# Kernel optimization log

Hardware: AMD Instinct MI355X
Metric: run time of the kernel (lower is better)

## Reference

```python
import jax, jax.numpy as jnp
import numpy as np

INPUT_DIM = 16
LW = 128          # layerwidth
NB_LAYERS = 4
NB_X = 4096
NB_THETA = 128
PARAM_COUNT = INPUT_DIM * LW + LW + (NB_LAYERS - 1) * (LW * LW + LW) + LW + 1  # 51841


def setup_inputs() -> dict:
    k1, k2 = jax.random.split(jax.random.key(0))
    x = jax.random.normal(k1, (NB_X, INPUT_DIM), dtype=jnp.float32)
    theta = jax.random.normal(k2, (NB_THETA, PARAM_COUNT), dtype=jnp.float32)
    return {"x": x, "theta": theta}


def reference(x, theta):
    # x: [nb_x, input_dim], theta: [nb_theta, param_count]
    t = theta.shape[0]
    off = 0
    # first layer: W0 [t, LW, INPUT_DIM], b0 [t, LW]
    W0 = theta[:, off:off + INPUT_DIM * LW].reshape(t, LW, INPUT_DIM); off += INPUT_DIM * LW
    b0 = theta[:, off:off + LW]; off += LW
    h = jnp.tanh(jnp.einsum('thi,xi->txh', W0, x) + b0[:, None, :])  # [t, nb_x, LW]
    # hidden layers
    for _ in range(NB_LAYERS - 1):
        W = theta[:, off:off + LW * LW].reshape(t, LW, LW); off += LW * LW
        b = theta[:, off:off + LW]; off += LW
        h = jnp.tanh(jnp.einsum('tho,txo->txh', W, h) + b[:, None, :])
    # output layer: Wl [t, LW], bl [t, 1]
    Wl = theta[:, off:off + LW]; off += LW
    bl = theta[:, off:off + 1]
    out = jnp.einsum('th,txh->tx', Wl, h)[..., None] + bl[:, None, :]  # [t, nb_x, 1]
    return out
```

## Files before the change

kernel.cpp:

```cpp
#include <hip/hip_runtime.h>


#define IND      16
#define LWD      128
#define THREADS  256
#define PARAMS   51841

#define WS_L0    12582912
#define WS_X     (WS_L0 + 128 * 8192)
#define WS_TOTAL (WS_X + 32 * 8192)

#define LDS_W    0
#define LDS_B    32768
#define LDS_WL   (32768 + 1536)
#define LDS_SZ   (32768 + 1536 + 520)

typedef _Float16 f16x8 __attribute__((ext_vector_type(8)));
typedef _Float16 f16x4 __attribute__((ext_vector_type(4)));
typedef float    f32x16 __attribute__((ext_vector_type(16)));
typedef float    f32x4v __attribute__((ext_vector_type(4)));

union U4 { unsigned u[4]; f16x8 v; };

__device__ __forceinline__ float fast_tanh(float v) {
    float e = __builtin_amdgcn_exp2f(v * 2.8853900817779268f);
    return 1.0f - 2.0f * __builtin_amdgcn_rcpf(e + 1.0f);
}
__device__ __forceinline__ unsigned pkf16(float a, float b) {
    unsigned short ua = __builtin_bit_cast(unsigned short, (_Float16)a);
    unsigned short ub = __builtin_bit_cast(unsigned short, (_Float16)b);
    return (unsigned)ua | ((unsigned)ub << 16);
}
#define MFMA(A, B, C) __builtin_amdgcn_mfma_f32_32x32x16_f16((A), (B), (C), 0, 0, 0)

__device__ __forceinline__ void gload16(const void* g, void* l) {
    __builtin_amdgcn_global_load_lds(
        (const __attribute__((address_space(1))) void*)g,
        (__attribute__((address_space(3))) void*)l, 16, 0, 0);
}

__device__ __forceinline__ void conv8(const float* __restrict__ s, char* hidst, char* lodst) {
    float v[8];
    *reinterpret_cast<float4*>(v)     = *reinterpret_cast<const float4*>(s);
    *reinterpret_cast<float4*>(v + 4) = *reinterpret_cast<const float4*>(s + 4);
    f16x8 hi, lo;
#pragma unroll
    for (int i = 0; i < 8; ++i) {
        hi[i] = (_Float16)v[i];
        lo[i] = (_Float16)(v[i] - (float)hi[i]);
    }
    *reinterpret_cast<f16x8*>(hidst) = hi;
    *reinterpret_cast<f16x8*>(lodst) = lo;
}

__global__ __launch_bounds__(256)
void prep_kernel(const float* __restrict__ theta, const float* __restrict__ xin,
                 char* __restrict__ ws)
{
    const int b = blockIdx.x, tid = threadIdx.x;
    if (b < 3072) {
        const int t = b / 24, rem = b % 24, li = rem >> 3, hblk = rem & 7;
        const int h  = hblk * 16 + (tid >> 4);
        const int kc = (tid >> 1) & 7, kh = tid & 1;
        const float* src = theta + (size_t)t * PARAMS + 2176 + li * 16512
                         + h * 128 + kc * 16 + kh * 8;
        float v[8];
        *reinterpret_cast<float4*>(v)     = *reinterpret_cast<const float4*>(src);
        *reinterpret_cast<float4*>(v + 4) = *reinterpret_cast<const float4*>(src + 4);
        f16x8 p;
#pragma unroll
        for (int i = 0; i < 8; ++i) p[i] = (_Float16)v[i];
        char* img = ws + ((size_t)(t * 3 + li) << 15);
        *reinterpret_cast<f16x8*>(img + ((h >> 5) * 8 + kc) * 1024
                                      + (kh * 32 + (h & 31)) * 16) = p;
    } else if (b < 3136) {
        const int gid = (b - 3072) * 256 + tid;
        const int t = gid >> 7, h = gid & 127;
        const float* src = theta + (size_t)t * PARAMS + h * IND;
        char* dst = ws + WS_L0 + (size_t)t * 8192 + h * 32;
        conv8(src,     dst,      dst + 4096);
        conv8(src + 8, dst + 16, dst + 4096 + 16);
    } else {
        const int row = (b - 3136) * 256 + tid;
        const float* src = xin + (size_t)row * IND;
        char* dst = ws + WS_X + (size_t)(row >> 7) * 8192 + (row & 127) * 32;
        conv8(src,     dst,      dst + 4096);
        conv8(src + 8, dst + 16, dst + 4096 + 16);
    }
}

__global__ __launch_bounds__(THREADS, 3)
void mlp_main(const float* __restrict__ theta, const char* __restrict__ ws,
              float* __restrict__ out)
{
    __shared__ __align__(16) char sL[LDS_SZ];

    const int tid = threadIdx.x, bid = blockIdx.x;
    const int sw  = (bid & 7) * 512 + (bid >> 3);
    const int t   = sw >> 5, xt = sw & 31;
    const float* __restrict__ th = theta + (size_t)t * PARAMS;
    const int lane = tid & 63, w = tid >> 6, r31 = lane & 31, khalf = lane >> 5;
    const int bpa  = (lane ^ 32) << 2;

    {
        const char* img = ws + ((size_t)(t * 3) << 15);
#pragma unroll
        for (int c = 0; c < 8; ++c)
            gload16(img + (w + c * 4) * 1024 + lane * 16, sL + (w + c * 4) * 1024);
    }
    for (int k = tid; k < 513; k += THREADS) {
        float v = (k < 384) ? th[2176 + (k >> 7) * 16512 + 16384 + (k & 127)]
                            : th[51712 + (k - 384)];
        *reinterpret_cast<float*>(sL + LDS_B + k * 4) = v;
    }

    f32x16 acc[4];
    {
        const char* w0i = ws + WS_L0 + (size_t)t  * 8192;
        const char* xi  = ws + WS_X  + (size_t)xt * 8192;
        const int ro = r31 * 32 + khalf * 16;
        const f16x8 B0h = *reinterpret_cast<const f16x8*>(xi + w * 1024 + ro);
        const f16x8 B0l = *reinterpret_cast<const f16x8*>(xi + 4096 + w * 1024 + ro);
#pragma unroll
        for (int tt = 0; tt < 4; ++tt) {
#pragma unroll
            for (int g = 0; g < 4; ++g) {
                const float4 bv = *reinterpret_cast<const float4*>(
                    th + 2048 + tt * 32 + g * 8 + khalf * 4);
                acc[tt][4 * g + 0] = bv.x; acc[tt][4 * g + 1] = bv.y;
                acc[tt][4 * g + 2] = bv.z; acc[tt][4 * g + 3] = bv.w;
            }
            const f16x8 Ah = *reinterpret_cast<const f16x8*>(w0i + tt * 1024 + ro);
            const f16x8 Al = *reinterpret_cast<const f16x8*>(w0i + 4096 + tt * 1024 + ro);
            acc[tt] = MFMA(Al, B0h, acc[tt]);
            acc[tt] = MFMA(Ah, B0l, acc[tt]);
            acc[tt] = MFMA(Ah, B0h, acc[tt]);
        }
    }

    f16x8 Bf[8];
    auto activate_pack = [&]() {
        unsigned P0[16], P1[16];
#pragma unroll
        for (int tt = 0; tt < 4; ++tt)
#pragma unroll
            for (int g = 0; g < 4; ++g) {
                const float v0 = fast_tanh(acc[tt][4 * g + 0]);
                const float v1 = fast_tanh(acc[tt][4 * g + 1]);
                const float v2 = fast_tanh(acc[tt][4 * g + 2]);
                const float v3 = fast_tanh(acc[tt][4 * g + 3]);
                P0[tt * 4 + g] = pkf16(v0, v1);
                P1[tt * 4 + g] = pkf16(v2, v3);
            }
#pragma unroll
        for (int kc = 0; kc < 8; ++kc) {
            const unsigned s0 = khalf ? P0[2 * kc] : P0[2 * kc + 1];
            const unsigned s1 = khalf ? P1[2 * kc] : P1[2 * kc + 1];
            const unsigned r0 = (unsigned)__builtin_amdgcn_ds_bpermute(bpa, (int)s0);
            const unsigned r1 = (unsigned)__builtin_amdgcn_ds_bpermute(bpa, (int)s1);
            U4 u;
            u.u[0] = khalf ? r0 : P0[2 * kc];
            u.u[1] = khalf ? r1 : P1[2 * kc];
            u.u[2] = khalf ? P0[2 * kc + 1] : r0;
            u.u[3] = khalf ? P1[2 * kc + 1] : r1;
            Bf[kc] = u.v;
        }
    };
    activate_pack();
    __syncthreads();

#pragma unroll
    for (int l = 1; l <= 3; ++l) {
#pragma unroll
        for (int tt = 0; tt < 4; ++tt)
#pragma unroll
            for (int g = 0; g < 4; ++g) {
                const f32x4v bv = *reinterpret_cast<const f32x4v*>(
                    sL + LDS_B + (l - 1) * 512 + (tt * 32 + g * 8) * 4 + khalf * 16);
                acc[tt][4 * g + 0] = bv[0]; acc[tt][4 * g + 1] = bv[1];
                acc[tt][4 * g + 2] = bv[2]; acc[tt][4 * g + 3] = bv[3];
            }
#pragma unroll
        for (int kc = 0; kc < 8; ++kc)
#pragma unroll
            for (int tt = 0; tt < 4; ++tt) {
                const f16x8 a = *reinterpret_cast<const f16x8*>(
                    sL + (tt * 8 + kc) * 1024 + lane * 16);
                acc[tt] = MFMA(a, Bf[kc], acc[tt]);
            }
        if (l < 3) {
            __syncthreads();
            const char* img = ws + ((size_t)(t * 3 + l) << 15);
#pragma unroll
            for (int c = 0; c < 8; ++c)
                gload16(img + (w + c * 4) * 1024 + lane * 16, sL + (w + c * 4) * 1024);
            activate_pack();
            __syncthreads();
        }
    }

    float s = 0.0f;
#pragma unroll
    for (int tt = 0; tt < 4; ++tt)
#pragma unroll
        for (int g = 0; g < 4; ++g) {
            const f32x4v wv = *reinterpret_cast<const f32x4v*>(
                sL + LDS_WL + (tt * 32 + g * 8) * 4 + khalf * 16);
#pragma unroll
            for (int q = 0; q < 4; ++q)
                s = fmaf(fast_tanh(acc[tt][4 * g + q]), wv[q], s);
        }
    const float sp = __builtin_bit_cast(float,
        __builtin_amdgcn_ds_bpermute(bpa, __builtin_bit_cast(int, s)));
    const float res = s + sp + *reinterpret_cast<const float*>(sL + LDS_WL + 512);
    if (!khalf) out[(size_t)t * 4096 + xt * 128 + w * 32 + r31] = res;
}

__global__ __launch_bounds__(THREADS, 1)
void mlp_kernel_fb(const float* __restrict__ xin,
                   const float* __restrict__ theta,
                   float* __restrict__ out)
{
    __shared__ __align__(16) _Float16 sH   [128 * LWD];
    __shared__ __align__(16) _Float16 sWhi [LWD * LWD];
    __shared__ __align__(16) _Float16 sWlo [LWD * LWD];
    __shared__ __align__(16) _Float16 sX0hi[128 * IND];
    __shared__ __align__(16) _Float16 sX0lo[128 * IND];
    __shared__ __align__(16) _Float16 sW0hi[LWD * IND];
    __shared__ __align__(16) _Float16 sW0lo[LWD * IND];
    __shared__ float sB[2][LWD];
    __shared__ float sWl[LWD + 1];

    const int tid = threadIdx.x;
    const int bid = blockIdx.x;
    const int sw  = (bid & 7) * 512 + (bid >> 3);
    const int t   = sw >> 5;
    const int xt  = sw & 31;
    const float* __restrict__ th = theta + (size_t)t * PARAMS;
    const float* __restrict__ xg = xin   + (size_t)xt * (128 * IND);

#pragma unroll
    for (int j = 0; j < 2; ++j) {
        const int flat = j * 1024 + tid * 4;
        const float4 v = *reinterpret_cast<const float4*>(xg + flat);
        _Float16 h0 = (_Float16)v.x, h1 = (_Float16)v.y, h2 = (_Float16)v.z, h3 = (_Float16)v.w;
        f16x4 ph = {h0, h1, h2, h3};
        f16x4 pl = {(_Float16)(v.x - (float)h0), (_Float16)(v.y - (float)h1),
                    (_Float16)(v.z - (float)h2), (_Float16)(v.w - (float)h3)};
        *reinterpret_cast<f16x4*>(&sX0hi[flat]) = ph;
        *reinterpret_cast<f16x4*>(&sX0lo[flat]) = pl;
    }
#pragma unroll
    for (int j = 0; j < 2; ++j) {
        const int flat = j * 1024 + tid * 4;
        const float a0 = th[flat], a1 = th[flat + 1], a2 = th[flat + 2], a3 = th[flat + 3];
        _Float16 h0 = (_Float16)a0, h1 = (_Float16)a1, h2 = (_Float16)a2, h3 = (_Float16)a3;
        f16x4 ph = {h0, h1, h2, h3};
        f16x4 pl = {(_Float16)(a0 - (float)h0), (_Float16)(a1 - (float)h1),
                    (_Float16)(a2 - (float)h2), (_Float16)(a3 - (float)h3)};
        *reinterpret_cast<f16x4*>(&sW0hi[flat]) = ph;
        *reinterpret_cast<f16x4*>(&sW0lo[flat]) = pl;
    }
    if (tid < LWD) sB[0][tid] = th[IND * LWD + tid];
    __syncthreads();

    const int lane  = tid & 63;
    const int w     = tid >> 6;
    const int r31   = lane & 31;
    const int khalf = lane >> 5;
    const int hb    = (w >> 1) * 64;
    const int xb    = (w & 1) * 64;
    const int hA0 = hb + r31,  hA1 = hb + 32 + r31;
    const int xB0 = xb + r31,  xB1 = xb + 32 + r31;
    const int swzA0 = (hA0 & 15) << 4, swzA1 = (hA1 & 15) << 4;
    const int swzB0 = (xB0 & 15) << 4, swzB1 = (xB1 & 15) << 4;

    f32x16 acc[2][2];

    {
        const int kb = khalf * 16;
        f16x8 ah[2], al[2], bh[2], bl[2];
        ah[0] = *reinterpret_cast<const f16x8*>((const char*)sW0hi + hA0 * 32 + kb);
        ah[1] = *reinterpret_cast<const f16x8*>((const char*)sW0hi + hA1 * 32 + kb);
        al[0] = *reinterpret_cast<const f16x8*>((const char*)sW0lo + hA0 * 32 + kb);
        al[1] = *reinterpret_cast<const f16x8*>((const char*)sW0lo + hA1 * 32 + kb);
        bh[0] = *reinterpret_cast<const f16x8*>((const char*)sX0hi + xB0 * 32 + kb);
        bh[1] = *reinterpret_cast<const f16x8*>((const char*)sX0hi + xB1 * 32 + kb);
        bl[0] = *reinterpret_cast<const f16x8*>((const char*)sX0lo + xB0 * 32 + kb);
        bl[1] = *reinterpret_cast<const f16x8*>((const char*)sX0lo + xB1 * 32 + kb);
#pragma unroll
        for (int tt = 0; tt < 2; ++tt)
#pragma unroll
            for (int tx = 0; tx < 2; ++tx) {
                f32x16 a;
#pragma unroll
                for (int i = 0; i < 16; ++i) a[i] = 0.0f;
                a = MFMA(al[tt], bh[tx], a);
                a = MFMA(ah[tt], bl[tx], a);
                a = MFMA(ah[tt], bh[tx], a);
                acc[tt][tx] = a;
            }
    }

    auto epilogue = [&](const float* __restrict__ bb) {
#pragma unroll
        for (int tt = 0; tt < 2; ++tt)
#pragma unroll
            for (int tx = 0; tx < 2; ++tx) {
                const int xw  = xb + tx * 32 + r31;
                const int swz = (xw & 15) << 4;
#pragma unroll
                for (int g = 0; g < 4; ++g) {
                    const int hbase = hb + tt * 32 + g * 8 + khalf * 4;
                    f16x4 pk;
#pragma unroll
                    for (int q = 0; q < 4; ++q) {
                        const float v = acc[tt][tx][g * 4 + q] + bb[hbase + q];
                        pk[q] = (_Float16)(1.0f - 2.0f * __builtin_amdgcn_rcpf(
                            __builtin_amdgcn_exp2f(v * 2.8853900817779268f) + 1.0f));
                    }
                    *reinterpret_cast<f16x4*>((char*)sH + xw * 256 + ((hbase * 2) ^ swz)) = pk;
                }
            }
    };

    for (int l = 0; l < 3; ++l) {
        __syncthreads();
        const float* __restrict__ wsrc = th + 2176 + l * 16512;
#pragma unroll
        for (int j = 0; j < 16; ++j) {
            const int flat = j * 1024 + tid * 4;
            const int hrow = flat >> 7;
            const int o    = flat & 127;
            const float a0 = wsrc[flat], a1 = wsrc[flat + 1], a2 = wsrc[flat + 2], a3 = wsrc[flat + 3];
            _Float16 h0 = (_Float16)a0, h1 = (_Float16)a1, h2 = (_Float16)a2, h3 = (_Float16)a3;
            f16x4 ph = {h0, h1, h2, h3};
            f16x4 pl = {(_Float16)(a0 - (float)h0), (_Float16)(a1 - (float)h1),
                        (_Float16)(a2 - (float)h2), (_Float16)(a3 - (float)h3)};
            const int boff = hrow * 256 + ((o * 2) ^ ((hrow & 15) << 4));
            *reinterpret_cast<f16x4*>((char*)sWhi + boff) = ph;
            *reinterpret_cast<f16x4*>((char*)sWlo + boff) = pl;
        }
        if (tid < LWD) sB[(l + 1) & 1][tid] = wsrc[LWD * LWD + tid];
        if (l == 2) {
            if (tid < LWD) sWl[tid] = th[51712 + tid];
            if (tid == LWD) sWl[LWD] = th[51840];
        }

        epilogue(sB[l & 1]);
        __syncthreads();

#pragma unroll
        for (int tt = 0; tt < 2; ++tt)
#pragma unroll
            for (int tx = 0; tx < 2; ++tx)
#pragma unroll
                for (int i = 0; i < 16; ++i) acc[tt][tx][i] = 0.0f;
#pragma unroll
        for (int kc = 0; kc < 8; ++kc) {
            const int kb = kc * 32 + khalf * 16;
            f16x8 ah[2], al[2], bv[2];
            ah[0] = *reinterpret_cast<const f16x8*>((const char*)sWhi + hA0 * 256 + (kb ^ swzA0));
            ah[1] = *reinterpret_cast<const f16x8*>((const char*)sWhi + hA1 * 256 + (kb ^ swzA1));
            al[0] = *reinterpret_cast<const f16x8*>((const char*)sWlo + hA0 * 256 + (kb ^ swzA0));
            al[1] = *reinterpret_cast<const f16x8*>((const char*)sWlo + hA1 * 256 + (kb ^ swzA1));
            bv[0] = *reinterpret_cast<const f16x8*>((const char*)sH   + xB0 * 256 + (kb ^ swzB0));
            bv[1] = *reinterpret_cast<const f16x8*>((const char*)sH   + xB1 * 256 + (kb ^ swzB1));
#pragma unroll
            for (int tt = 0; tt < 2; ++tt)
#pragma unroll
                for (int tx = 0; tx < 2; ++tx) {
                    acc[tt][tx] = MFMA(al[tt], bv[tx], acc[tt][tx]);
                    acc[tt][tx] = MFMA(ah[tt], bv[tx], acc[tt][tx]);
                }
        }
    }

    __syncthreads();
    epilogue(sB[1]);
    __syncthreads();

    if (tid < 128) {
        const int r   = tid;
        const int swz = (r & 15) << 4;
        float s = 0.0f;
#pragma unroll
        for (int c = 0; c < 16; ++c) {
            const int hc = (c + r) & 15;
            const f16x8 hv = *reinterpret_cast<const f16x8*>(
                (const char*)sH + r * 256 + ((hc * 16) ^ swz));
#pragma unroll
            for (int q = 0; q < 8; ++q) s += (float)hv[q] * sWl[hc * 8 + q];
        }
        out[(size_t)t * 4096 + (size_t)xt * 128 + r] = s + sWl[LWD];
    }
}

extern "C" void kernel_launch(void* const* d_in, const int* in_sizes, int n_in,
                              void* d_out, int out_size, void* d_ws, size_t ws_size,
                              hipStream_t stream)
{
    const float* x     = (const float*)d_in[0];
    const float* theta = (const float*)d_in[1];
    float* out = (float*)d_out;

    if (ws_size >= (size_t)WS_TOTAL) {
        prep_kernel<<<dim3(3152), dim3(256), 0, stream>>>(theta, x, (char*)d_ws);
        mlp_main<<<dim3(4096), dim3(THREADS), 0, stream>>>(theta, (const char*)d_ws, out);
    } else {
        mlp_kernel_fb<<<dim3(4096), dim3(THREADS), 0, stream>>>(x, theta, out);
    }
}
```

Measured before the change: 105.3 us.

## Cut register pressure with per-tile packing, permlane32 swap, and higher occupancy

Activation packing now runs per output tile, so only four packed registers per half are live at a time instead of sixteen. Where the builtin is available, the cross-half exchange uses permlane32_swap instead of ds_bpermute through LDS. The MFMA loop is reordered to finish one tile's K-chain before starting the next, is wrapped in s_setprio to favour the matrix phase, and the launch bounds ask for four blocks per CU instead of three. The aim is more waves resident and fewer LDS permute round trips, at the risk of register spills under the tighter bound and longer serial dependency chains on each accumulator.

Measured after the change: 105.2 us. No clear change (-0.1%).

```diff
diff --git a/kernel.cpp b/kernel.cpp
--- a/kernel.cpp
+++ b/kernel.cpp
@@ -10,7 +10,6 @@
 #define WS_X     (WS_L0 + 128 * 8192)
 #define WS_TOTAL (WS_X + 32 * 8192)
 
-#define LDS_W    0
 #define LDS_B    32768
 #define LDS_WL   (32768 + 1536)
 #define LDS_SZ   (32768 + 1536 + 520)
@@ -19,6 +18,7 @@
 typedef _Float16 f16x4 __attribute__((ext_vector_type(4)));
 typedef float    f32x16 __attribute__((ext_vector_type(16)));
 typedef float    f32x4v __attribute__((ext_vector_type(4)));
+typedef unsigned u32x2  __attribute__((ext_vector_type(2)));
 
 union U4 { unsigned u[4]; f16x8 v; };
 
@@ -89,7 +89,7 @@
     }
 }
 
-__global__ __launch_bounds__(THREADS, 3)
+__global__ __launch_bounds__(THREADS, 4)
 void mlp_main(const float* __restrict__ theta, const char* __restrict__ ws,
               float* __restrict__ out)
 {
@@ -140,30 +140,40 @@
 
     f16x8 Bf[8];
     auto activate_pack = [&]() {
-        unsigned P0[16], P1[16];
-#pragma unroll
-        for (int tt = 0; tt < 4; ++tt)
+#pragma unroll
+        for (int tt = 0; tt < 4; ++tt) {
+            unsigned P0[4], P1[4];
 #pragma unroll
             for (int g = 0; g < 4; ++g) {
                 const float v0 = fast_tanh(acc[tt][4 * g + 0]);
                 const float v1 = fast_tanh(acc[tt][4 * g + 1]);
                 const float v2 = fast_tanh(acc[tt][4 * g + 2]);
                 const float v3 = fast_tanh(acc[tt][4 * g + 3]);
-                P0[tt * 4 + g] = pkf16(v0, v1);
-                P1[tt * 4 + g] = pkf16(v2, v3);
-            }
-#pragma unroll
-        for (int kc = 0; kc < 8; ++kc) {
-            const unsigned s0 = khalf ? P0[2 * kc] : P0[2 * kc + 1];
-            const unsigned s1 = khalf ? P1[2 * kc] : P1[2 * kc + 1];
-            const unsigned r0 = (unsigned)__builtin_amdgcn_ds_bpermute(bpa, (int)s0);
-            const unsigned r1 = (unsigned)__builtin_amdgcn_ds_bpermute(bpa, (int)s1);
-            U4 u;
-            u.u[0] = khalf ? r0 : P0[2 * kc];
-            u.u[1] = khalf ? r1 : P1[2 * kc];
-            u.u[2] = khalf ? P0[2 * kc + 1] : r0;
-            u.u[3] = khalf ? P1[2 * kc + 1] : r1;
-            Bf[kc] = u.v;
+                P0[g] = pkf16(v0, v1);
+                P1[g] = pkf16(v2, v3);
+            }
+#pragma unroll
+            for (int j = 0; j < 2; ++j) {
+#if __has_builtin(__builtin_amdgcn_permlane32_swap)
+                const u32x2 r0 = __builtin_amdgcn_permlane32_swap(
+                    P0[2 * j], P0[2 * j + 1], false, false);
+                const u32x2 r1 = __builtin_amdgcn_permlane32_swap(
+                    P1[2 * j], P1[2 * j + 1], false, false);
+                U4 u;
+                u.u[0] = r0[0]; u.u[1] = r1[0]; u.u[2] = r0[1]; u.u[3] = r1[1];
+#else
+                const unsigned s0 = khalf ? P0[2 * j] : P0[2 * j + 1];
+                const unsigned s1 = khalf ? P1[2 * j] : P1[2 * j + 1];
+                const unsigned q0 = (unsigned)__builtin_amdgcn_ds_bpermute(bpa, (int)s0);
+                const unsigned q1 = (unsigned)__builtin_amdgcn_ds_bpermute(bpa, (int)s1);
+                U4 u;
+                u.u[0] = khalf ? q0 : P0[2 * j];
+                u.u[1] = khalf ? q1 : P1[2 * j];
+                u.u[2] = khalf ? P0[2 * j + 1] : q0;
+                u.u[3] = khalf ? P1[2 * j + 1] : q1;
+#endif
+                Bf[2 * tt + j] = u.v;
+            }
         }
     };
     activate_pack();
@@ -171,8 +181,9 @@
 
 #pragma unroll
     for (int l = 1; l <= 3; ++l) {
-#pragma unroll
-        for (int tt = 0; tt < 4; ++tt)
+        __builtin_amdgcn_s_setprio(1);
+#pragma unroll
+        for (int tt = 0; tt < 4; ++tt) {
 #pragma unroll
             for (int g = 0; g < 4; ++g) {
                 const f32x4v bv = *reinterpret_cast<const f32x4v*>(
@@ -181,13 +192,13 @@
                 acc[tt][4 * g + 2] = bv[2]; acc[tt][4 * g + 3] = bv[3];
             }
 #pragma unroll
-        for (int kc = 0; kc < 8; ++kc)
-#pragma unroll
-            for (int tt = 0; tt < 4; ++tt) {
+            for (int kc = 0; kc < 8; ++kc) {
                 const f16x8 a = *reinterpret_cast<const f16x8*>(
                     sL + (tt * 8 + kc) * 1024 + lane * 16);
                 acc[tt] = MFMA(a, Bf[kc], acc[tt]);
             }
+        }
+        __builtin_amdgcn_s_setprio(0);
         if (l < 3) {
             __syncthreads();
             const char* img = ws + ((size_t)(t * 3 + l) << 15);
```
